# Kernel tuning notes

Hardware: AMD Instinct MI355X
Metric: run time of the kernel (lower is better)

Reference implementation:

```python
import jax, jax.numpy as jnp
import numpy as np

DIM = 768
N_HEADS = 12
HEAD_DIM = DIM // N_HEADS
BATCH = 2
SEQ = 4096


def setup_inputs() -> dict:
    key = jax.random.key(0)
    ks = jax.random.split(key, 9)
    s = 1.0 / np.sqrt(DIM)
    return {
        "x": jax.random.normal(ks[0], (BATCH, SEQ, DIM), dtype=jnp.float32),
        "Wq": jax.random.normal(ks[1], (DIM, DIM), dtype=jnp.float32) * s,
        "bq": jax.random.normal(ks[2], (DIM,), dtype=jnp.float32) * s,
        "Wk": jax.random.normal(ks[3], (DIM, DIM), dtype=jnp.float32) * s,
        "bk": jax.random.normal(ks[4], (DIM,), dtype=jnp.float32) * s,
        "Wv": jax.random.normal(ks[5], (DIM, DIM), dtype=jnp.float32) * s,
        "bv": jax.random.normal(ks[6], (DIM,), dtype=jnp.float32) * s,
        "Wo": jax.random.normal(ks[7], (DIM, DIM), dtype=jnp.float32) * s,
        "bo": jax.random.normal(ks[8], (DIM,), dtype=jnp.float32) * s,
    }


def reference(x, Wq, bq, Wk, bk, Wv, bv, Wo, bo):
    B, S, D = x.shape
    scale = 1.0 / np.sqrt(HEAD_DIM).astype(np.float32)
    # projections: [B,S,D] -> [B,H,S,Hd]
    def split_heads(t):
        return t.reshape(B, S, N_HEADS, HEAD_DIM).transpose(0, 2, 1, 3)
    q = split_heads(x @ Wq + bq)
    k = split_heads(x @ Wk + bk)
    v = split_heads(x @ Wv + bv)
    # full score matrix [B,H,S,S] as in the original (memory-bound)
    scores = jnp.einsum("bhqd,bhkd->bhqk", q, k) * scale
    attn = jax.nn.softmax(scores, axis=-1)
    out = jnp.einsum("bhqk,bhkd->bhqd", attn, v)
    out = out.transpose(0, 2, 1, 3).reshape(B, S, D)
    return out @ Wo + bo
```

## Files before the change

kernel.cpp:

```cpp
#include <hip/hip_runtime.h>
#include <hip/hip_bf16.h>
#include <math.h>

#define D_MODEL 768
#define NH 12
#define HD 64
#define BATCH 2
#define SEQ 4096
#define NROWS (BATCH * SEQ)

#define QSCALE 0.18033688011112042f

typedef __attribute__((ext_vector_type(8))) short short8;
typedef __attribute__((ext_vector_type(4))) short short4v;
typedef __attribute__((ext_vector_type(4))) float f32x4;
typedef __attribute__((ext_vector_type(16))) float f32x16;
typedef __attribute__((ext_vector_type(4))) unsigned int uint4v;

__device__ inline unsigned short f2bf(float f) {
    __hip_bfloat16 h = __float2bfloat16(f);
    return *reinterpret_cast<unsigned short*>(&h);
}

__device__ __forceinline__ unsigned int cvtpk_bf16(float lo, float hi) {
    unsigned int d;
    asm("v_cvt_pk_bf16_f32 %0, %1, %2" : "=v"(d) : "v"(lo), "v"(hi));
    return d;
}

__device__ __forceinline__ short8 u4_as_s8(uint4v u) {
    return *reinterpret_cast<short8*>(&u);
}

__device__ __forceinline__ void async_ld16(const unsigned short* g, unsigned short* l) {
    __builtin_amdgcn_global_load_lds(
        (const __attribute__((address_space(1))) void*)g,
        (__attribute__((address_space(3))) void*)l, 16, 0, 0);
}

__global__ __launch_bounds__(256) void convert_x_k(
    const float* __restrict__ x, unsigned short* __restrict__ xb)
{
    size_t i = ((size_t)blockIdx.x * 256 + threadIdx.x) * 8;
    float4 a = *(const float4*)(x + i);
    float4 b = *(const float4*)(x + i + 4);
    short8 o;
    o[0] = (short)f2bf(a.x); o[1] = (short)f2bf(a.y);
    o[2] = (short)f2bf(a.z); o[3] = (short)f2bf(a.w);
    o[4] = (short)f2bf(b.x); o[5] = (short)f2bf(b.y);
    o[6] = (short)f2bf(b.z); o[7] = (short)f2bf(b.w);
    *(short8*)(xb + i) = o;
}

__global__ __launch_bounds__(256) void convert_wt_k(
    const float* __restrict__ Wq, const float* __restrict__ Wk,
    const float* __restrict__ Wv, const float* __restrict__ Wo,
    unsigned short* __restrict__ wt)
{
    const float* W = (blockIdx.z == 0) ? Wq : (blockIdx.z == 1) ? Wk
                   : (blockIdx.z == 2) ? Wv : Wo;
    unsigned short* dst = wt + (size_t)blockIdx.z * D_MODEL * D_MODEL;
    __shared__ float tile[64][65];
    const int k0 = blockIdx.x * 64, n0 = blockIdx.y * 64;
    const int t = threadIdx.x;
    const int r = t >> 2, seg = t & 3;
    const float* src = W + (size_t)(k0 + r) * D_MODEL + n0 + seg * 16;
    #pragma unroll
    for (int i = 0; i < 4; ++i) {
        float4 v = *(const float4*)(src + i * 4);
        tile[r][seg * 16 + i * 4 + 0] = v.x;
        tile[r][seg * 16 + i * 4 + 1] = v.y;
        tile[r][seg * 16 + i * 4 + 2] = v.z;
        tile[r][seg * 16 + i * 4 + 3] = v.w;
    }
    __syncthreads();
    unsigned short* d = dst + (size_t)(n0 + r) * D_MODEL + k0 + seg * 16;
    short8 o0, o1;
    #pragma unroll
    for (int j = 0; j < 8; ++j) o0[j] = (short)f2bf(tile[seg * 16 + j][r]);
    #pragma unroll
    for (int j = 0; j < 8; ++j) o1[j] = (short)f2bf(tile[seg * 16 + 8 + j][r]);
    *(short8*)(d) = o0;
    *(short8*)(d + 8) = o1;
}

__global__ __launch_bounds__(256) void qkv_mfma_k(
    const unsigned short* __restrict__ xb,
    const unsigned short* __restrict__ wt,
    const float* __restrict__ bq, const float* __restrict__ bk,
    const float* __restrict__ bv,
    unsigned short* __restrict__ qb,
    unsigned short* __restrict__ kb,
    unsigned short* __restrict__ vtb)
{
    __shared__ unsigned short As[128][64];
    __shared__ unsigned short Bs[64][64];
    const int z = blockIdx.z;
    const unsigned short* Wt = wt + (size_t)z * D_MODEL * D_MODEL;
    const float* bias = (z == 0) ? bq : (z == 1) ? bk : bv;
    const int t = threadIdx.x;
    const int w = t >> 6, lane = t & 63, quad = lane >> 4, col = lane & 15;
    const int r0 = blockIdx.x * 128;
    const int c0 = blockIdx.y * 64;

    f32x4 acc[2][4] = {};

    for (int kk = 0; kk < D_MODEL; kk += 64) {
        __syncthreads();
        #pragma unroll
        for (int j = 0; j < 4; ++j) {
            int c = (w * 4 + j) * 64 + lane;
            async_ld16(xb + (size_t)(r0 + (c >> 3)) * D_MODEL + kk + (c & 7) * 8,
                       &As[0][0] + (size_t)c * 8);
        }
        #pragma unroll
        for (int j = 0; j < 2; ++j) {
            int c = (w * 2 + j) * 64 + lane;
            async_ld16(Wt + (size_t)(c0 + (c >> 3)) * D_MODEL + kk + (c & 7) * 8,
                       &Bs[0][0] + (size_t)c * 8);
        }
        __syncthreads();
        #pragma unroll
        for (int ks = 0; ks < 2; ++ks) {
            short8 af[2], bf[4];
            af[0] = *(const short8*)&As[w * 32 + col][ks * 32 + quad * 8];
            af[1] = *(const short8*)&As[w * 32 + 16 + col][ks * 32 + quad * 8];
            #pragma unroll
            for (int nt = 0; nt < 4; ++nt)
                bf[nt] = *(const short8*)&Bs[nt * 16 + col][ks * 32 + quad * 8];
            #pragma unroll
            for (int mt = 0; mt < 2; ++mt)
                #pragma unroll
                for (int nt = 0; nt < 4; ++nt)
                    acc[mt][nt] = __builtin_amdgcn_mfma_f32_16x16x32_bf16(
                        af[mt], bf[nt], acc[mt][nt], 0, 0, 0);
        }
    }

    const int h = blockIdx.y;
    #pragma unroll
    for (int nt = 0; nt < 4; ++nt) {
        const float bv_ = bias[c0 + nt * 16 + col];
        const int hd = nt * 16 + col;
        #pragma unroll
        for (int mt = 0; mt < 2; ++mt) {
            #pragma unroll
            for (int reg = 0; reg < 4; ++reg) {
                int r = r0 + w * 32 + mt * 16 + quad * 4 + reg;
                int b = r >> 12, s = r & (SEQ - 1);
                float val = acc[mt][nt][reg] + bv_;
                size_t bh = (size_t)(b * NH + h);
                if (z == 0)
                    qb[(bh * SEQ + s) * HD + hd] = f2bf(val * QSCALE);
                else if (z == 1)
                    kb[(bh * SEQ + s) * HD + hd] = f2bf(val);
                else
                    vtb[(bh * HD + hd) * SEQ + s] = f2bf(val);
            }
        }
    }
}

__global__ __launch_bounds__(256) void out_mfma_k(
    const unsigned short* __restrict__ ab,
    const unsigned short* __restrict__ wot,
    const float* __restrict__ bo,
    float* __restrict__ out)
{
    __shared__ unsigned short As[128][64];
    __shared__ unsigned short Bs[64][64];
    const int t = threadIdx.x;
    const int w = t >> 6, lane = t & 63, quad = lane >> 4, col = lane & 15;
    const int r0 = blockIdx.x * 128;
    const int c0 = blockIdx.y * 64;

    f32x4 acc[2][4] = {};

    for (int kk = 0; kk < D_MODEL; kk += 64) {
        __syncthreads();
        #pragma unroll
        for (int j = 0; j < 4; ++j) {
            int c = (w * 4 + j) * 64 + lane;
            async_ld16(ab + (size_t)(r0 + (c >> 3)) * D_MODEL + kk + (c & 7) * 8,
                       &As[0][0] + (size_t)c * 8);
        }
        #pragma unroll
        for (int j = 0; j < 2; ++j) {
            int c = (w * 2 + j) * 64 + lane;
            async_ld16(wot + (size_t)(c0 + (c >> 3)) * D_MODEL + kk + (c & 7) * 8,
                       &Bs[0][0] + (size_t)c * 8);
        }
        __syncthreads();
        #pragma unroll
        for (int ks = 0; ks < 2; ++ks) {
            short8 af[2], bf[4];
            af[0] = *(const short8*)&As[w * 32 + col][ks * 32 + quad * 8];
            af[1] = *(const short8*)&As[w * 32 + 16 + col][ks * 32 + quad * 8];
            #pragma unroll
            for (int nt = 0; nt < 4; ++nt)
                bf[nt] = *(const short8*)&Bs[nt * 16 + col][ks * 32 + quad * 8];
            #pragma unroll
            for (int mt = 0; mt < 2; ++mt)
                #pragma unroll
                for (int nt = 0; nt < 4; ++nt)
                    acc[mt][nt] = __builtin_amdgcn_mfma_f32_16x16x32_bf16(
                        af[mt], bf[nt], acc[mt][nt], 0, 0, 0);
        }
    }

    #pragma unroll
    for (int nt = 0; nt < 4; ++nt) {
        const float bv_ = bo[c0 + nt * 16 + col];
        #pragma unroll
        for (int mt = 0; mt < 2; ++mt) {
            #pragma unroll
            for (int reg = 0; reg < 4; ++reg) {
                int r = r0 + w * 32 + mt * 16 + quad * 4 + reg;
                out[(size_t)r * D_MODEL + c0 + nt * 16 + col] = acc[mt][nt][reg] + bv_;
            }
        }
    }
}

__global__ __launch_bounds__(256) void flash_mfma_k(
    const unsigned short* __restrict__ qb,
    const unsigned short* __restrict__ kb,
    const unsigned short* __restrict__ vtb,
    unsigned short* __restrict__ ab)
{
    __shared__ unsigned short Ks[64][66];
    __shared__ unsigned short Vts[64][66];

    const int t = threadIdx.x;
    const int w = t >> 6, lane = t & 63;
    const int l31 = lane & 31, hi = lane >> 5;
    const int q0 = blockIdx.x * 128;
    const int h = blockIdx.y, b = blockIdx.z;
    const size_t bh = (size_t)b * NH + h;
    const unsigned short* qg = qb + bh * SEQ * HD;
    const unsigned short* kg = kb + bh * SEQ * HD;
    const unsigned short* vg = vtb + bh * HD * SEQ;

    short8 qf[4];
    {
        const unsigned short* src = qg + (size_t)(q0 + w * 32 + l31) * HD + hi * 8;
        #pragma unroll
        for (int ks = 0; ks < 4; ++ks)
            qf[ks] = *(const short8*)(src + ks * 16);
    }

    f32x16 oacc[2] = {};
    float lsum = 0.f;
    const int srow = lane, sseg = w;

    short8 kr0, kr1, vr0, vr1;
    {
        const unsigned short* kp = kg + (size_t)srow * HD + sseg * 16;
        kr0 = *(const short8*)(kp);
        kr1 = *(const short8*)(kp + 8);
        const unsigned short* vp = vg + (size_t)srow * SEQ + sseg * 16;
        vr0 = *(const short8*)(vp);
        vr1 = *(const short8*)(vp + 8);
    }

    for (int kt = 0; kt < SEQ; kt += 64) {
        __syncthreads();
        *(short8*)&Ks[srow][sseg * 16]      = kr0;
        *(short8*)&Ks[srow][sseg * 16 + 8]  = kr1;
        *(short8*)&Vts[srow][sseg * 16]     = vr0;
        *(short8*)&Vts[srow][sseg * 16 + 8] = vr1;
        if (kt + 64 < SEQ) {
            const unsigned short* kp = kg + (size_t)(kt + 64 + srow) * HD + sseg * 16;
            kr0 = *(const short8*)(kp);
            kr1 = *(const short8*)(kp + 8);
            const unsigned short* vp = vg + (size_t)srow * SEQ + kt + 64 + sseg * 16;
            vr0 = *(const short8*)(vp);
            vr1 = *(const short8*)(vp + 8);
        }
        __syncthreads();

        short8 pf[4];
        #pragma unroll
        for (int kti = 0; kti < 2; ++kti) {
            f32x16 s = {};
            __builtin_amdgcn_s_setprio(1);
            #pragma unroll
            for (int ks = 0; ks < 4; ++ks) {
                short8 kf = *(const short8*)&Ks[kti * 32 + l31][ks * 16 + hi * 8];
                s = __builtin_amdgcn_mfma_f32_32x32x16_bf16(kf, qf[ks], s, 0, 0, 0);
            }
            __builtin_amdgcn_s_setprio(0);
            float p[16];
            #pragma unroll
            for (int r = 0; r < 16; ++r)
                p[r] = __builtin_amdgcn_exp2f(s[r]);
            lsum += (((p[0] + p[1]) + (p[2] + p[3])) + ((p[4] + p[5]) + (p[6] + p[7])))
                  + (((p[8] + p[9]) + (p[10] + p[11])) + ((p[12] + p[13]) + (p[14] + p[15])));
            unsigned int c01 = cvtpk_bf16(p[0],  p[1]);
            unsigned int c45 = cvtpk_bf16(p[4],  p[5]);
            unsigned int c23 = cvtpk_bf16(p[2],  p[3]);
            unsigned int c67 = cvtpk_bf16(p[6],  p[7]);
            unsigned int c89 = cvtpk_bf16(p[8],  p[9]);
            unsigned int cCD = cvtpk_bf16(p[12], p[13]);
            unsigned int cAB = cvtpk_bf16(p[10], p[11]);
            unsigned int cEF = cvtpk_bf16(p[14], p[15]);
            auto r0 = __builtin_amdgcn_permlane32_swap((int)c01, (int)c45, false, false);
            auto r1 = __builtin_amdgcn_permlane32_swap((int)c23, (int)c67, false, false);
            auto r2 = __builtin_amdgcn_permlane32_swap((int)c89, (int)cCD, false, false);
            auto r3 = __builtin_amdgcn_permlane32_swap((int)cAB, (int)cEF, false, false);
            uint4v u0, u1;
            u0[0] = (unsigned int)r0[0]; u0[1] = (unsigned int)r1[0];
            u0[2] = (unsigned int)r0[1]; u0[3] = (unsigned int)r1[1];
            u1[0] = (unsigned int)r2[0]; u1[1] = (unsigned int)r3[0];
            u1[2] = (unsigned int)r2[1]; u1[3] = (unsigned int)r3[1];
            pf[kti * 2 + 0] = u4_as_s8(u0);
            pf[kti * 2 + 1] = u4_as_s8(u1);
        }

        __builtin_amdgcn_s_setprio(1);
        #pragma unroll
        for (int ks = 0; ks < 4; ++ks) {
            short8 pfk = pf[ks];
            #pragma unroll
            for (int dt = 0; dt < 2; ++dt) {
                short8 vf = *(const short8*)&Vts[dt * 32 + l31][ks * 16 + hi * 8];
                oacc[dt] = __builtin_amdgcn_mfma_f32_32x32x16_bf16(
                    vf, pfk, oacc[dt], 0, 0, 0);
            }
        }
        __builtin_amdgcn_s_setprio(0);
    }

    lsum += __shfl_xor(lsum, 32);
    float inv = 1.0f / lsum;
    int s = q0 + w * 32 + l31;
    unsigned short* dst = ab + ((size_t)b * SEQ + s) * D_MODEL + h * HD;
    #pragma unroll
    for (int dt = 0; dt < 2; ++dt) {
        #pragma unroll
        for (int rq = 0; rq < 4; ++rq) {
            short4v o4;
            o4[0] = (short)f2bf(oacc[dt][rq * 4 + 0] * inv);
            o4[1] = (short)f2bf(oacc[dt][rq * 4 + 1] * inv);
            o4[2] = (short)f2bf(oacc[dt][rq * 4 + 2] * inv);
            o4[3] = (short)f2bf(oacc[dt][rq * 4 + 3] * inv);
            *(short4v*)(dst + dt * 32 + rq * 8 + hi * 4) = o4;
        }
    }
}

extern "C" void kernel_launch(void* const* d_in, const int* in_sizes, int n_in,
                              void* d_out, int out_size, void* d_ws, size_t ws_size,
                              hipStream_t stream)
{
    const float* x  = (const float*)d_in[0];
    const float* Wq = (const float*)d_in[1];
    const float* bq = (const float*)d_in[2];
    const float* Wk = (const float*)d_in[3];
    const float* bk = (const float*)d_in[4];
    const float* Wv = (const float*)d_in[5];
    const float* bv = (const float*)d_in[6];
    const float* Wo = (const float*)d_in[7];
    const float* bo = (const float*)d_in[8];
    float* out = (float*)d_out;

    const size_t n_x  = (size_t)NROWS * D_MODEL;
    const size_t n_w  = (size_t)D_MODEL * D_MODEL;
    unsigned short* xb  = (unsigned short*)d_ws;
    unsigned short* wt  = xb + n_x;
    unsigned short* qb  = wt + 4 * n_w;
    unsigned short* kb  = qb + n_x;
    unsigned short* vtb = kb + n_x;
    unsigned short* ab  = vtb + n_x;
    const size_t need = ((size_t)4 * n_x + 4 * n_w + n_x) * sizeof(unsigned short);
    if (ws_size < need) return;

    convert_x_k<<<dim3((int)(n_x / 2048)), 256, 0, stream>>>(x, xb);
    convert_wt_k<<<dim3(12, 12, 4), 256, 0, stream>>>(Wq, Wk, Wv, Wo, wt);
    qkv_mfma_k<<<dim3(NROWS / 128, D_MODEL / 64, 3), 256, 0, stream>>>(
        xb, wt, bq, bk, bv, qb, kb, vtb);
    flash_mfma_k<<<dim3(SEQ / 128, NH, BATCH), 256, 0, stream>>>(qb, kb, vtb, ab);
    out_mfma_k<<<dim3(NROWS / 128, D_MODEL / 64), 256, 0, stream>>>(
        ab, wt + 3 * n_w, bo, out);
}
```

Baseline: 306.3 us.

## Process two 32-row query tiles per wave in flash attention

The flash attention kernel now runs 2 waves per block instead of 4, and each wave handles 64 query rows as two 32-row MFMA tiles. Each K/V fragment read from LDS is reused for both tiles, which halves LDS traffic per MFMA and gives more independent MFMA chains to interleave with the exp work. In exchange, register pressure per thread roughly doubles (two accumulator sets and two Q fragment sets) and each block has fewer waves to hide barrier and load latency. The cooperative tile load is adjusted so each thread copies 32 columns.

```diff
diff --git a/kernel.cpp b/kernel.cpp
--- a/kernel.cpp
+++ b/kernel.cpp
@@ -222,7 +222,37 @@
     }
 }
 
-__global__ __launch_bounds__(256) void flash_mfma_k(
+__device__ __forceinline__ void softmax_pack(
+    const f32x16& s, float& lsum, short8& pf0, short8& pf1)
+{
+    float p[16];
+    #pragma unroll
+    for (int r = 0; r < 16; ++r)
+        p[r] = __builtin_amdgcn_exp2f(s[r]);
+    lsum += (((p[0] + p[1]) + (p[2] + p[3])) + ((p[4] + p[5]) + (p[6] + p[7])))
+          + (((p[8] + p[9]) + (p[10] + p[11])) + ((p[12] + p[13]) + (p[14] + p[15])));
+    unsigned int c01 = cvtpk_bf16(p[0],  p[1]);
+    unsigned int c45 = cvtpk_bf16(p[4],  p[5]);
+    unsigned int c23 = cvtpk_bf16(p[2],  p[3]);
+    unsigned int c67 = cvtpk_bf16(p[6],  p[7]);
+    unsigned int c89 = cvtpk_bf16(p[8],  p[9]);
+    unsigned int cCD = cvtpk_bf16(p[12], p[13]);
+    unsigned int cAB = cvtpk_bf16(p[10], p[11]);
+    unsigned int cEF = cvtpk_bf16(p[14], p[15]);
+    auto r0 = __builtin_amdgcn_permlane32_swap((int)c01, (int)c45, false, false);
+    auto r1 = __builtin_amdgcn_permlane32_swap((int)c23, (int)c67, false, false);
+    auto r2 = __builtin_amdgcn_permlane32_swap((int)c89, (int)cCD, false, false);
+    auto r3 = __builtin_amdgcn_permlane32_swap((int)cAB, (int)cEF, false, false);
+    uint4v u0, u1;
+    u0[0] = (unsigned int)r0[0]; u0[1] = (unsigned int)r1[0];
+    u0[2] = (unsigned int)r0[1]; u0[3] = (unsigned int)r1[1];
+    u1[0] = (unsigned int)r2[0]; u1[1] = (unsigned int)r3[0];
+    u1[2] = (unsigned int)r2[1]; u1[3] = (unsigned int)r3[1];
+    pf0 = u4_as_s8(u0);
+    pf1 = u4_as_s8(u1);
+}
+
+__global__ __launch_bounds__(128, 2) void flash_mfma_k(
     const unsigned short* __restrict__ qb,
     const unsigned short* __restrict__ kb,
     const unsigned short* __restrict__ vtb,
@@ -241,110 +271,105 @@
     const unsigned short* kg = kb + bh * SEQ * HD;
     const unsigned short* vg = vtb + bh * HD * SEQ;
 
-    short8 qf[4];
+    short8 qfA[4], qfB[4];
     {
-        const unsigned short* src = qg + (size_t)(q0 + w * 32 + l31) * HD + hi * 8;
-        #pragma unroll
-        for (int ks = 0; ks < 4; ++ks)
-            qf[ks] = *(const short8*)(src + ks * 16);
-    }
-
-    f32x16 oacc[2] = {};
-    float lsum = 0.f;
+        const unsigned short* srcA = qg + (size_t)(q0 + w * 64 + l31) * HD + hi * 8;
+        const unsigned short* srcB = srcA + (size_t)32 * HD;
+        #pragma unroll
+        for (int ks = 0; ks < 4; ++ks) {
+            qfA[ks] = *(const short8*)(srcA + ks * 16);
+            qfB[ks] = *(const short8*)(srcB + ks * 16);
+        }
+    }
+
+    f32x16 oaccA[2] = {}, oaccB[2] = {};
+    float lsumA = 0.f, lsumB = 0.f;
     const int srow = lane, sseg = w;
 
-    short8 kr0, kr1, vr0, vr1;
+    short8 kr[4], vr[4];
     {
-        const unsigned short* kp = kg + (size_t)srow * HD + sseg * 16;
-        kr0 = *(const short8*)(kp);
-        kr1 = *(const short8*)(kp + 8);
-        const unsigned short* vp = vg + (size_t)srow * SEQ + sseg * 16;
-        vr0 = *(const short8*)(vp);
-        vr1 = *(const short8*)(vp + 8);
+        const unsigned short* kp = kg + (size_t)srow * HD + sseg * 32;
+        const unsigned short* vp = vg + (size_t)srow * SEQ + sseg * 32;
+        #pragma unroll
+        for (int c = 0; c < 4; ++c) {
+            kr[c] = *(const short8*)(kp + c * 8);
+            vr[c] = *(const short8*)(vp + c * 8);
+        }
     }
 
     for (int kt = 0; kt < SEQ; kt += 64) {
         __syncthreads();
-        *(short8*)&Ks[srow][sseg * 16]      = kr0;
-        *(short8*)&Ks[srow][sseg * 16 + 8]  = kr1;
-        *(short8*)&Vts[srow][sseg * 16]     = vr0;
-        *(short8*)&Vts[srow][sseg * 16 + 8] = vr1;
+        #pragma unroll
+        for (int c = 0; c < 4; ++c) {
+            *(short8*)&Ks[srow][sseg * 32 + c * 8]  = kr[c];
+            *(short8*)&Vts[srow][sseg * 32 + c * 8] = vr[c];
+        }
         if (kt + 64 < SEQ) {
-            const unsigned short* kp = kg + (size_t)(kt + 64 + srow) * HD + sseg * 16;
-            kr0 = *(const short8*)(kp);
-            kr1 = *(const short8*)(kp + 8);
-            const unsigned short* vp = vg + (size_t)srow * SEQ + kt + 64 + sseg * 16;
-            vr0 = *(const short8*)(vp);
-            vr1 = *(const short8*)(vp + 8);
-        }
-        __syncthreads();
-
-        short8 pf[4];
+            const unsigned short* kp = kg + (size_t)(kt + 64 + srow) * HD + sseg * 32;
+            const unsigned short* vp = vg + (size_t)srow * SEQ + kt + 64 + sseg * 32;
+            #pragma unroll
+            for (int c = 0; c < 4; ++c) {
+                kr[c] = *(const short8*)(kp + c * 8);
+                vr[c] = *(const short8*)(vp + c * 8);
+            }
+        }
+        __syncthreads();
+
+        short8 pfA[4], pfB[4];
         #pragma unroll
         for (int kti = 0; kti < 2; ++kti) {
-            f32x16 s = {};
+            f32x16 sA = {}, sB = {};
             __builtin_amdgcn_s_setprio(1);
             #pragma unroll
             for (int ks = 0; ks < 4; ++ks) {
                 short8 kf = *(const short8*)&Ks[kti * 32 + l31][ks * 16 + hi * 8];
-                s = __builtin_amdgcn_mfma_f32_32x32x16_bf16(kf, qf[ks], s, 0, 0, 0);
+                sA = __builtin_amdgcn_mfma_f32_32x32x16_bf16(kf, qfA[ks], sA, 0, 0, 0);
+                sB = __builtin_amdgcn_mfma_f32_32x32x16_bf16(kf, qfB[ks], sB, 0, 0, 0);
             }
             __builtin_amdgcn_s_setprio(0);
-            float p[16];
-            #pragma unroll
-            for (int r = 0; r < 16; ++r)
-                p[r] = __builtin_amdgcn_exp2f(s[r]);
-            lsum += (((p[0] + p[1]) + (p[2] + p[3])) + ((p[4] + p[5]) + (p[6] + p[7])))
-                  + (((p[8] + p[9]) + (p[10] + p[11])) + ((p[12] + p[13]) + (p[14] + p[15])));
-            unsigned int c01 = cvtpk_bf16(p[0],  p[1]);
-            unsigned int c45 = cvtpk_bf16(p[4],  p[5]);
-            unsigned int c23 = cvtpk_bf16(p[2],  p[3]);
-            unsigned int c67 = cvtpk_bf16(p[6],  p[7]);
-            unsigned int c89 = cvtpk_bf16(p[8],  p[9]);
-            unsigned int cCD = cvtpk_bf16(p[12], p[13]);
-            unsigned int cAB = cvtpk_bf16(p[10], p[11]);
-            unsigned int cEF = cvtpk_bf16(p[14], p[15]);
-            auto r0 = __builtin_amdgcn_permlane32_swap((int)c01, (int)c45, false, false);
-            auto r1 = __builtin_amdgcn_permlane32_swap((int)c23, (int)c67, false, false);
-            auto r2 = __builtin_amdgcn_permlane32_swap((int)c89, (int)cCD, false, false);
-            auto r3 = __builtin_amdgcn_permlane32_swap((int)cAB, (int)cEF, false, false);
-            uint4v u0, u1;
-            u0[0] = (unsigned int)r0[0]; u0[1] = (unsigned int)r1[0];
-            u0[2] = (unsigned int)r0[1]; u0[3] = (unsigned int)r1[1];
-            u1[0] = (unsigned int)r2[0]; u1[1] = (unsigned int)r3[0];
-            u1[2] = (unsigned int)r2[1]; u1[3] = (unsigned int)r3[1];
-            pf[kti * 2 + 0] = u4_as_s8(u0);
-            pf[kti * 2 + 1] = u4_as_s8(u1);
+            softmax_pack(sA, lsumA, pfA[kti * 2 + 0], pfA[kti * 2 + 1]);
+            softmax_pack(sB, lsumB, pfB[kti * 2 + 0], pfB[kti * 2 + 1]);
         }
 
         __builtin_amdgcn_s_setprio(1);
         #pragma unroll
         for (int ks = 0; ks < 4; ++ks) {
-            short8 pfk = pf[ks];
+            short8 pkA = pfA[ks], pkB = pfB[ks];
             #pragma unroll
             for (int dt = 0; dt < 2; ++dt) {
                 short8 vf = *(const short8*)&Vts[dt * 32 + l31][ks * 16 + hi * 8];
-                oacc[dt] = __builtin_amdgcn_mfma_f32_32x32x16_bf16(
-                    vf, pfk, oacc[dt], 0, 0, 0);
+                oaccA[dt] = __builtin_amdgcn_mfma_f32_32x32x16_bf16(
+                    vf, pkA, oaccA[dt], 0, 0, 0);
+                oaccB[dt] = __builtin_amdgcn_mfma_f32_32x32x16_bf16(
+                    vf, pkB, oaccB[dt], 0, 0, 0);
             }
         }
         __builtin_amdgcn_s_setprio(0);
     }
 
-    lsum += __shfl_xor(lsum, 32);
-    float inv = 1.0f / lsum;
-    int s = q0 + w * 32 + l31;
-    unsigned short* dst = ab + ((size_t)b * SEQ + s) * D_MODEL + h * HD;
+    lsumA += __shfl_xor(lsumA, 32);
+    lsumB += __shfl_xor(lsumB, 32);
+    float invA = 1.0f / lsumA;
+    float invB = 1.0f / lsumB;
+    int sA_row = q0 + w * 64 + l31;
+    unsigned short* dstA = ab + ((size_t)b * SEQ + sA_row) * D_MODEL + h * HD;
+    unsigned short* dstB = dstA + (size_t)32 * D_MODEL;
     #pragma unroll
     for (int dt = 0; dt < 2; ++dt) {
         #pragma unroll
         for (int rq = 0; rq < 4; ++rq) {
             short4v o4;
-            o4[0] = (short)f2bf(oacc[dt][rq * 4 + 0] * inv);
-            o4[1] = (short)f2bf(oacc[dt][rq * 4 + 1] * inv);
-            o4[2] = (short)f2bf(oacc[dt][rq * 4 + 2] * inv);
-            o4[3] = (short)f2bf(oacc[dt][rq * 4 + 3] * inv);
-            *(short4v*)(dst + dt * 32 + rq * 8 + hi * 4) = o4;
+            o4[0] = (short)f2bf(oaccA[dt][rq * 4 + 0] * invA);
+            o4[1] = (short)f2bf(oaccA[dt][rq * 4 + 1] * invA);
+            o4[2] = (short)f2bf(oaccA[dt][rq * 4 + 2] * invA);
+            o4[3] = (short)f2bf(oaccA[dt][rq * 4 + 3] * invA);
+            *(short4v*)(dstA + dt * 32 + rq * 8 + hi * 4) = o4;
+            short4v o4b;
+            o4b[0] = (short)f2bf(oaccB[dt][rq * 4 + 0] * invB);
+            o4b[1] = (short)f2bf(oaccB[dt][rq * 4 + 1] * invB);
+            o4b[2] = (short)f2bf(oaccB[dt][rq * 4 + 2] * invB);
+            o4b[3] = (short)f2bf(oaccB[dt][rq * 4 + 3] * invB);
+            *(short4v*)(dstB + dt * 32 + rq * 8 + hi * 4) = o4b;
         }
     }
 }
@@ -379,7 +404,7 @@
     convert_wt_k<<<dim3(12, 12, 4), 256, 0, stream>>>(Wq, Wk, Wv, Wo, wt);
     qkv_mfma_k<<<dim3(NROWS / 128, D_MODEL / 64, 3), 256, 0, stream>>>(
         xb, wt, bq, bk, bv, qb, kb, vtb);
-    flash_mfma_k<<<dim3(SEQ / 128, NH, BATCH), 256, 0, stream>>>(qb, kb, vtb, ab);
+    flash_mfma_k<<<dim3(SEQ / 128, NH, BATCH), 128, 0, stream>>>(qb, kb, vtb, ab);
     out_mfma_k<<<dim3(NROWS / 128, D_MODEL / 64), 256, 0, stream>>>(
         ab, wt + 3 * n_w, bo, out);
 }
```

Result: no change. 304.6 us (-0.5%).

## Split flash attention over two KV halves with a separate combine kernel

Applied to the files above, without the earlier changes.

Adds a split-KV path: each attention block processes half of the key sequence and writes unnormalized fp32 partial outputs and row sums to workspace. A new combine kernel adds the two halves, normalizes, and writes bf16 attention output. This doubles the grid (768 to 1536 blocks) to improve CU occupancy and load balance, at the cost of extra fp32 partial traffic and one more launch. No running max is kept, so adding the halves directly is valid, and the path is used only when the workspace is large enough.

```diff
diff --git a/kernel.cpp b/kernel.cpp
--- a/kernel.cpp
+++ b/kernel.cpp
@@ -222,6 +222,179 @@
     }
 }
 
+__device__ __forceinline__ void softmax_pack(
+    const f32x16& s, float& lsum, short8& pf0, short8& pf1)
+{
+    float p[16];
+    #pragma unroll
+    for (int r = 0; r < 16; ++r)
+        p[r] = __builtin_amdgcn_exp2f(s[r]);
+    lsum += (((p[0] + p[1]) + (p[2] + p[3])) + ((p[4] + p[5]) + (p[6] + p[7])))
+          + (((p[8] + p[9]) + (p[10] + p[11])) + ((p[12] + p[13]) + (p[14] + p[15])));
+    unsigned int c01 = cvtpk_bf16(p[0],  p[1]);
+    unsigned int c45 = cvtpk_bf16(p[4],  p[5]);
+    unsigned int c23 = cvtpk_bf16(p[2],  p[3]);
+    unsigned int c67 = cvtpk_bf16(p[6],  p[7]);
+    unsigned int c89 = cvtpk_bf16(p[8],  p[9]);
+    unsigned int cCD = cvtpk_bf16(p[12], p[13]);
+    unsigned int cAB = cvtpk_bf16(p[10], p[11]);
+    unsigned int cEF = cvtpk_bf16(p[14], p[15]);
+    auto r0 = __builtin_amdgcn_permlane32_swap((int)c01, (int)c45, false, false);
+    auto r1 = __builtin_amdgcn_permlane32_swap((int)c23, (int)c67, false, false);
+    auto r2 = __builtin_amdgcn_permlane32_swap((int)c89, (int)cCD, false, false);
+    auto r3 = __builtin_amdgcn_permlane32_swap((int)cAB, (int)cEF, false, false);
+    uint4v u0, u1;
+    u0[0] = (unsigned int)r0[0]; u0[1] = (unsigned int)r1[0];
+    u0[2] = (unsigned int)r0[1]; u0[3] = (unsigned int)r1[1];
+    u1[0] = (unsigned int)r2[0]; u1[1] = (unsigned int)r3[0];
+    u1[2] = (unsigned int)r2[1]; u1[3] = (unsigned int)r3[1];
+    pf0 = u4_as_s8(u0);
+    pf1 = u4_as_s8(u1);
+}
+
+__device__ __forceinline__ void flash_core(
+    const unsigned short* __restrict__ qg,
+    const unsigned short* __restrict__ kg,
+    const unsigned short* __restrict__ vg,
+    int q0, int kt0, int nk, int w, int lane,
+    unsigned short (*Ks)[66], unsigned short (*Vts)[66],
+    f32x16 oacc[2], float& lsum)
+{
+    const int l31 = lane & 31, hi = lane >> 5;
+    short8 qf[4];
+    {
+        const unsigned short* src = qg + (size_t)(q0 + w * 32 + l31) * HD + hi * 8;
+        #pragma unroll
+        for (int ks = 0; ks < 4; ++ks)
+            qf[ks] = *(const short8*)(src + ks * 16);
+    }
+
+    const int srow = lane, sseg = w;
+    short8 kr0, kr1, vr0, vr1;
+    {
+        const unsigned short* kp = kg + (size_t)(kt0 + srow) * HD + sseg * 16;
+        kr0 = *(const short8*)(kp);
+        kr1 = *(const short8*)(kp + 8);
+        const unsigned short* vp = vg + (size_t)srow * SEQ + kt0 + sseg * 16;
+        vr0 = *(const short8*)(vp);
+        vr1 = *(const short8*)(vp + 8);
+    }
+
+    for (int kt = kt0; kt < kt0 + nk; kt += 64) {
+        __syncthreads();
+        *(short8*)&Ks[srow][sseg * 16]      = kr0;
+        *(short8*)&Ks[srow][sseg * 16 + 8]  = kr1;
+        *(short8*)&Vts[srow][sseg * 16]     = vr0;
+        *(short8*)&Vts[srow][sseg * 16 + 8] = vr1;
+        if (kt + 64 < kt0 + nk) {
+            const unsigned short* kp = kg + (size_t)(kt + 64 + srow) * HD + sseg * 16;
+            kr0 = *(const short8*)(kp);
+            kr1 = *(const short8*)(kp + 8);
+            const unsigned short* vp = vg + (size_t)srow * SEQ + kt + 64 + sseg * 16;
+            vr0 = *(const short8*)(vp);
+            vr1 = *(const short8*)(vp + 8);
+        }
+        __syncthreads();
+
+        short8 pf[4];
+        #pragma unroll
+        for (int kti = 0; kti < 2; ++kti) {
+            f32x16 s = {};
+            __builtin_amdgcn_s_setprio(1);
+            #pragma unroll
+            for (int ks = 0; ks < 4; ++ks) {
+                short8 kf = *(const short8*)&Ks[kti * 32 + l31][ks * 16 + hi * 8];
+                s = __builtin_amdgcn_mfma_f32_32x32x16_bf16(kf, qf[ks], s, 0, 0, 0);
+            }
+            __builtin_amdgcn_s_setprio(0);
+            softmax_pack(s, lsum, pf[kti * 2 + 0], pf[kti * 2 + 1]);
+        }
+
+        __builtin_amdgcn_s_setprio(1);
+        #pragma unroll
+        for (int ks = 0; ks < 4; ++ks) {
+            short8 pfk = pf[ks];
+            #pragma unroll
+            for (int dt = 0; dt < 2; ++dt) {
+                short8 vf = *(const short8*)&Vts[dt * 32 + l31][ks * 16 + hi * 8];
+                oacc[dt] = __builtin_amdgcn_mfma_f32_32x32x16_bf16(
+                    vf, pfk, oacc[dt], 0, 0, 0);
+            }
+        }
+        __builtin_amdgcn_s_setprio(0);
+    }
+}
+
+__global__ __launch_bounds__(256) void flash_split_k(
+    const unsigned short* __restrict__ qb,
+    const unsigned short* __restrict__ kb,
+    const unsigned short* __restrict__ vtb,
+    float* __restrict__ opart,
+    float* __restrict__ lpart)
+{
+    __shared__ unsigned short Ks[64][66];
+    __shared__ unsigned short Vts[64][66];
+
+    const int t = threadIdx.x;
+    const int w = t >> 6, lane = t & 63;
+    const int l31 = lane & 31, hi = lane >> 5;
+    const int q0 = blockIdx.x * 128;
+    const int h = blockIdx.y;
+    const int b = blockIdx.z >> 1, half = blockIdx.z & 1;
+    const size_t bh = (size_t)b * NH + h;
+    const unsigned short* qg = qb + bh * SEQ * HD;
+    const unsigned short* kg = kb + bh * SEQ * HD;
+    const unsigned short* vg = vtb + bh * HD * SEQ;
+
+    f32x16 oacc[2] = {};
+    float lsum = 0.f;
+    flash_core(qg, kg, vg, q0, half * (SEQ / 2), SEQ / 2, w, lane, Ks, Vts,
+               oacc, lsum);
+
+    lsum += __shfl_xor(lsum, 32);
+    const size_t row = bh * SEQ + (q0 + w * 32 + l31);
+    float* ob = opart + ((size_t)half * NROWS * NH * 0
+                         + (size_t)half * (size_t)BATCH * NH * SEQ * HD)
+                      + row * HD;
+    if (hi == 0) lpart[(size_t)half * BATCH * NH * SEQ + row] = lsum;
+    #pragma unroll
+    for (int dt = 0; dt < 2; ++dt) {
+        #pragma unroll
+        for (int rq = 0; rq < 4; ++rq) {
+            f32x4 v;
+            v[0] = oacc[dt][rq * 4 + 0];
+            v[1] = oacc[dt][rq * 4 + 1];
+            v[2] = oacc[dt][rq * 4 + 2];
+            v[3] = oacc[dt][rq * 4 + 3];
+            *(f32x4*)(ob + dt * 32 + rq * 8 + hi * 4) = v;
+        }
+    }
+}
+
+__global__ __launch_bounds__(256) void combine_k(
+    const float* __restrict__ opart, const float* __restrict__ lpart,
+    unsigned short* __restrict__ ab)
+{
+    const size_t nO = (size_t)BATCH * NH * SEQ * HD;
+    size_t e = ((size_t)blockIdx.x * 256 + threadIdx.x) * 8;
+    size_t row = e >> 6;
+    int d0 = (int)(e & 63);
+    int bh = (int)(row >> 12), s = (int)(row & (SEQ - 1));
+    int b = bh / NH, h = bh - b * NH;
+    float inv = 1.0f / (lpart[row] + lpart[(size_t)BATCH * NH * SEQ + row]);
+    f32x4 a0 = *(const f32x4*)(opart + e);
+    f32x4 a1 = *(const f32x4*)(opart + e + 4);
+    f32x4 b0 = *(const f32x4*)(opart + nO + e);
+    f32x4 b1 = *(const f32x4*)(opart + nO + e + 4);
+    short8 o;
+    #pragma unroll
+    for (int j = 0; j < 4; ++j) {
+        o[j]     = (short)f2bf((a0[j] + b0[j]) * inv);
+        o[4 + j] = (short)f2bf((a1[j] + b1[j]) * inv);
+    }
+    *(short8*)(ab + ((size_t)(b * SEQ + s)) * D_MODEL + h * HD + d0) = o;
+}
+
 __global__ __launch_bounds__(256) void flash_mfma_k(
     const unsigned short* __restrict__ qb,
     const unsigned short* __restrict__ kb,
@@ -241,95 +414,9 @@
     const unsigned short* kg = kb + bh * SEQ * HD;
     const unsigned short* vg = vtb + bh * HD * SEQ;
 
-    short8 qf[4];
-    {
-        const unsigned short* src = qg + (size_t)(q0 + w * 32 + l31) * HD + hi * 8;
-        #pragma unroll
-        for (int ks = 0; ks < 4; ++ks)
-            qf[ks] = *(const short8*)(src + ks * 16);
-    }
-
     f32x16 oacc[2] = {};
     float lsum = 0.f;
-    const int srow = lane, sseg = w;
-
-    short8 kr0, kr1, vr0, vr1;
-    {
-        const unsigned short* kp = kg + (size_t)srow * HD + sseg * 16;
-        kr0 = *(const short8*)(kp);
-        kr1 = *(const short8*)(kp + 8);
-        const unsigned short* vp = vg + (size_t)srow * SEQ + sseg * 16;
-        vr0 = *(const short8*)(vp);
-        vr1 = *(const short8*)(vp + 8);
-    }
-
-    for (int kt = 0; kt < SEQ; kt += 64) {
-        __syncthreads();
-        *(short8*)&Ks[srow][sseg * 16]      = kr0;
-        *(short8*)&Ks[srow][sseg * 16 + 8]  = kr1;
-        *(short8*)&Vts[srow][sseg * 16]     = vr0;
-        *(short8*)&Vts[srow][sseg * 16 + 8] = vr1;
-        if (kt + 64 < SEQ) {
-            const unsigned short* kp = kg + (size_t)(kt + 64 + srow) * HD + sseg * 16;
-            kr0 = *(const short8*)(kp);
-            kr1 = *(const short8*)(kp + 8);
-            const unsigned short* vp = vg + (size_t)srow * SEQ + kt + 64 + sseg * 16;
-            vr0 = *(const short8*)(vp);
-            vr1 = *(const short8*)(vp + 8);
-        }
-        __syncthreads();
-
-        short8 pf[4];
-        #pragma unroll
-        for (int kti = 0; kti < 2; ++kti) {
-            f32x16 s = {};
-            __builtin_amdgcn_s_setprio(1);
-            #pragma unroll
-            for (int ks = 0; ks < 4; ++ks) {
-                short8 kf = *(const short8*)&Ks[kti * 32 + l31][ks * 16 + hi * 8];
-                s = __builtin_amdgcn_mfma_f32_32x32x16_bf16(kf, qf[ks], s, 0, 0, 0);
-            }
-            __builtin_amdgcn_s_setprio(0);
-            float p[16];
-            #pragma unroll
-            for (int r = 0; r < 16; ++r)
-                p[r] = __builtin_amdgcn_exp2f(s[r]);
-            lsum += (((p[0] + p[1]) + (p[2] + p[3])) + ((p[4] + p[5]) + (p[6] + p[7])))
-                  + (((p[8] + p[9]) + (p[10] + p[11])) + ((p[12] + p[13]) + (p[14] + p[15])));
-            unsigned int c01 = cvtpk_bf16(p[0],  p[1]);
-            unsigned int c45 = cvtpk_bf16(p[4],  p[5]);
-            unsigned int c23 = cvtpk_bf16(p[2],  p[3]);
-            unsigned int c67 = cvtpk_bf16(p[6],  p[7]);
-            unsigned int c89 = cvtpk_bf16(p[8],  p[9]);
-            unsigned int cCD = cvtpk_bf16(p[12], p[13]);
-            unsigned int cAB = cvtpk_bf16(p[10], p[11]);
-            unsigned int cEF = cvtpk_bf16(p[14], p[15]);
-            auto r0 = __builtin_amdgcn_permlane32_swap((int)c01, (int)c45, false, false);
-            auto r1 = __builtin_amdgcn_permlane32_swap((int)c23, (int)c67, false, false);
-            auto r2 = __builtin_amdgcn_permlane32_swap((int)c89, (int)cCD, false, false);
-            auto r3 = __builtin_amdgcn_permlane32_swap((int)cAB, (int)cEF, false, false);
-            uint4v u0, u1;
-            u0[0] = (unsigned int)r0[0]; u0[1] = (unsigned int)r1[0];
-            u0[2] = (unsigned int)r0[1]; u0[3] = (unsigned int)r1[1];
-            u1[0] = (unsigned int)r2[0]; u1[1] = (unsigned int)r3[0];
-            u1[2] = (unsigned int)r2[1]; u1[3] = (unsigned int)r3[1];
-            pf[kti * 2 + 0] = u4_as_s8(u0);
-            pf[kti * 2 + 1] = u4_as_s8(u1);
-        }
-
-        __builtin_amdgcn_s_setprio(1);
-        #pragma unroll
-        for (int ks = 0; ks < 4; ++ks) {
-            short8 pfk = pf[ks];
-            #pragma unroll
-            for (int dt = 0; dt < 2; ++dt) {
-                short8 vf = *(const short8*)&Vts[dt * 32 + l31][ks * 16 + hi * 8];
-                oacc[dt] = __builtin_amdgcn_mfma_f32_32x32x16_bf16(
-                    vf, pfk, oacc[dt], 0, 0, 0);
-            }
-        }
-        __builtin_amdgcn_s_setprio(0);
-    }
+    flash_core(qg, kg, vg, q0, 0, SEQ, w, lane, Ks, Vts, oacc, lsum);
 
     lsum += __shfl_xor(lsum, 32);
     float inv = 1.0f / lsum;
@@ -366,20 +453,31 @@
 
     const size_t n_x  = (size_t)NROWS * D_MODEL;
     const size_t n_w  = (size_t)D_MODEL * D_MODEL;
+    const size_t n_l  = (size_t)BATCH * NH * SEQ;
     unsigned short* xb  = (unsigned short*)d_ws;
     unsigned short* wt  = xb + n_x;
     unsigned short* qb  = wt + 4 * n_w;
     unsigned short* kb  = qb + n_x;
     unsigned short* vtb = kb + n_x;
     unsigned short* ab  = vtb + n_x;
-    const size_t need = ((size_t)4 * n_x + 4 * n_w + n_x) * sizeof(unsigned short);
+    float* opart = (float*)(ab + n_x);
+    float* lpart = opart + 2 * n_x;
+    const size_t need = ((size_t)5 * n_x + 4 * n_w) * sizeof(unsigned short);
+    const size_t need_split = need + (2 * n_x + 2 * n_l) * sizeof(float);
     if (ws_size < need) return;
 
     convert_x_k<<<dim3((int)(n_x / 2048)), 256, 0, stream>>>(x, xb);
     convert_wt_k<<<dim3(12, 12, 4), 256, 0, stream>>>(Wq, Wk, Wv, Wo, wt);
     qkv_mfma_k<<<dim3(NROWS / 128, D_MODEL / 64, 3), 256, 0, stream>>>(
         xb, wt, bq, bk, bv, qb, kb, vtb);
-    flash_mfma_k<<<dim3(SEQ / 128, NH, BATCH), 256, 0, stream>>>(qb, kb, vtb, ab);
+    if (ws_size >= need_split) {
+        flash_split_k<<<dim3(SEQ / 128, NH, BATCH * 2), 256, 0, stream>>>(
+            qb, kb, vtb, opart, lpart);
+        combine_k<<<dim3((int)(n_x / 2048)), 256, 0, stream>>>(opart, lpart, ab);
+    } else {
+        flash_mfma_k<<<dim3(SEQ / 128, NH, BATCH), 256, 0, stream>>>(
+            qb, kb, vtb, ab);
+    }
     out_mfma_k<<<dim3(NROWS / 128, D_MODEL / 64), 256, 0, stream>>>(
         ab, wt + 3 * n_w, bo, out);
 }
```

Result: slower. 601.9 us (+96.5%).
